# Optimization experiments

Hardware: AMD Instinct MI355X
Metric: run time of the kernel (lower is better)

Reference implementation:

```python
import jax, jax.numpy as jnp
import numpy as np

N_HEADS = 16


def setup_inputs() -> dict:
    key = jax.random.key(0)
    k1, k2, k3, k4 = jax.random.split(key, 4)
    b, s, d = 2, 2048, 1024
    x = jax.random.normal(k1, (b, s, d), dtype=jnp.float32)
    attn_B = jax.random.normal(k2, (b, N_HEADS, s, s), dtype=jnp.float32) * 0.02
    W_attn = jax.random.normal(k3, (d, 3 * d), dtype=jnp.float32) * (1.0 / np.sqrt(d))
    b_attn = jax.random.normal(k4, (3 * d,), dtype=jnp.float32) * 0.01
    return {"x": x, "attn_B": attn_B, "W_attn": W_attn, "b_attn": b_attn}


def reference(x, attn_B, W_attn, b_attn):
    b, s, d = x.shape
    h = N_HEADS
    hd = d // h
    qkv = x @ W_attn + b_attn                       # [b, s, 3d]
    Q, K, V = jnp.split(qkv, 3, axis=-1)
    # [b, s, d] -> [b, h, s, hd]
    Q = Q.reshape(b, s, h, hd).transpose(0, 2, 1, 3)
    K = K.reshape(b, s, h, hd).transpose(0, 2, 1, 3)
    V = V.reshape(b, s, h, hd).transpose(0, 2, 1, 3)
    scale = 1.0 / jnp.sqrt(jnp.asarray(hd, dtype=Q.dtype))
    scores = jnp.einsum("bhqk,bhsk->bhqs", Q, K) * scale   # [b, h, s, s]
    attn = jax.nn.softmax(scores, axis=-1) + attn_B          # post-softmax additive bias
    y = jnp.einsum("bhqs,bhsd->bhqd", attn, V)               # [b, h, s, hd]
    y = y.transpose(0, 2, 1, 3).reshape(b, s, d)
    return y
```

## Files before the change

### kernel.cpp

```cpp
#include <hip/hip_runtime.h>
#include <hip/hip_bf16.h>


typedef __attribute__((ext_vector_type(4))) float  f32x4;
typedef __attribute__((ext_vector_type(8))) short  bf16x8;
typedef __attribute__((ext_vector_type(4))) short  s16x4;

__device__ __forceinline__ short f2bf(float f) {
    __hip_bfloat16 h = __float2bfloat16(f);
    return __builtin_bit_cast(short, h);
}

__device__ __forceinline__ unsigned cvt_pk_bf16(float lo, float hi) {
    unsigned w;
    asm("v_cvt_pk_bf16_f32 %0, %1, %2" : "=v"(w) : "v"(lo), "v"(hi));
    return w;
}

__device__ __forceinline__ void gll16(const short* g, short* l) {
    __builtin_amdgcn_global_load_lds(
        (const __attribute__((address_space(1))) void*)g,
        (__attribute__((address_space(3))) void*)l, 16, 0, 0);
}

__global__ void conv_x_kernel(const float* __restrict__ x, short* __restrict__ xb) {
    int idx = blockIdx.x * 256 + threadIdx.x;
    f32x4 v = *reinterpret_cast<const f32x4*>(x + (size_t)idx * 4);
    s16x4 o;
    o[0] = f2bf(v[0]); o[1] = f2bf(v[1]); o[2] = f2bf(v[2]); o[3] = f2bf(v[3]);
    *reinterpret_cast<s16x4*>(xb + (size_t)idx * 4) = o;
}

__global__ void wtrans_kernel(const float* __restrict__ W, short* __restrict__ Wt) {
    __shared__ float tile[64][65];
    int kb = blockIdx.x, nb = blockIdx.y;
    int t = threadIdx.x;
    int c4 = (t & 15) * 4;
    int r0 = t >> 4;
#pragma unroll
    for (int rr = 0; rr < 4; ++rr) {
        int kl = r0 + rr * 16;
        f32x4 v = *reinterpret_cast<const f32x4*>(W + (size_t)(kb * 64 + kl) * 3072 + nb * 64 + c4);
        tile[kl][c4 + 0] = v[0]; tile[kl][c4 + 1] = v[1];
        tile[kl][c4 + 2] = v[2]; tile[kl][c4 + 3] = v[3];
    }
    __syncthreads();
#pragma unroll
    for (int rr = 0; rr < 4; ++rr) {
        int nl = r0 + rr * 16;
        s16x4 o;
#pragma unroll
        for (int i = 0; i < 4; ++i) o[i] = f2bf(tile[c4 + i][nl]);
        *reinterpret_cast<s16x4*>(Wt + (size_t)(nb * 64 + nl) * 1024 + kb * 64 + c4) = o;
    }
}

__global__ __launch_bounds__(256) void qkv_gemm_kernel(
    const short* __restrict__ xb, const short* __restrict__ Wt,
    const float* __restrict__ bias,
    short* __restrict__ Qo, short* __restrict__ Ko, short* __restrict__ Vo)
{
    __shared__ short As[128 * 64];
    __shared__ short Bs[128 * 64];
    int tid = threadIdx.x;
    int wave = tid >> 6, lane = tid & 63, g = lane >> 4, lr = lane & 15;
    int wr = wave >> 1, wc = wave & 1;
    int bm = blockIdx.x, bn = blockIdx.y;

    f32x4 acc[4][4];
#pragma unroll
    for (int a = 0; a < 4; ++a)
#pragma unroll
        for (int b = 0; b < 4; ++b) acc[a][b] = (f32x4){0.f, 0.f, 0.f, 0.f};

    for (int k0 = 0; k0 < 1024; k0 += 64) {
#pragma unroll
        for (int j = 0; j < 4; ++j) {
            int c = j * 256 + tid;
            int row = c >> 3, cc = c & 7;
            int scc = (cc ^ (row & 7)) * 8;
            gll16(xb + (size_t)(bm * 128 + row) * 1024 + k0 + scc,
                  &As[(j * 256 + wave * 64) * 8]);
            gll16(Wt + (size_t)(bn * 128 + row) * 1024 + k0 + scc,
                  &Bs[(j * 256 + wave * 64) * 8]);
        }
        __syncthreads();

        bf16x8 af[2][4], bfr[2][4];
#pragma unroll
        for (int mt = 0; mt < 4; ++mt) {
            int row = wr * 64 + mt * 16 + lr;
            af[0][mt] = *reinterpret_cast<const bf16x8*>(&As[row * 64 + (((g    ) ^ (lr & 7)) * 8)]);
            af[1][mt] = *reinterpret_cast<const bf16x8*>(&As[row * 64 + (((g + 4) ^ (lr & 7)) * 8)]);
        }
#pragma unroll
        for (int nt = 0; nt < 4; ++nt) {
            int row = wc * 64 + nt * 16 + lr;
            bfr[0][nt] = *reinterpret_cast<const bf16x8*>(&Bs[row * 64 + (((g    ) ^ (lr & 7)) * 8)]);
            bfr[1][nt] = *reinterpret_cast<const bf16x8*>(&Bs[row * 64 + (((g + 4) ^ (lr & 7)) * 8)]);
        }
#pragma unroll
        for (int mt = 0; mt < 4; ++mt)
#pragma unroll
            for (int nt = 0; nt < 4; ++nt) {
                acc[mt][nt] = __builtin_amdgcn_mfma_f32_16x16x32_bf16(af[0][mt], bfr[0][nt], acc[mt][nt], 0, 0, 0);
                acc[mt][nt] = __builtin_amdgcn_mfma_f32_16x16x32_bf16(af[1][mt], bfr[1][nt], acc[mt][nt], 0, 0, 0);
            }
        __syncthreads();
    }

#pragma unroll
    for (int nt = 0; nt < 4; ++nt) {
        int n = bn * 128 + wc * 64 + nt * 16 + lr;
        float bv = bias[n];
        int which = n >> 10;
        int h = (n >> 6) & 15;
        int dd = n & 63;
        short* base = (which == 0) ? Qo : (which == 1) ? Ko : Vo;
#pragma unroll
        for (int mt = 0; mt < 4; ++mt) {
#pragma unroll
            for (int r = 0; r < 4; ++r) {
                int m = bm * 128 + wr * 64 + mt * 16 + g * 4 + r;
                int bb = m >> 11, s = m & 2047;
                float v = acc[mt][nt][r] + bv;
                base[(((size_t)bb * 16 + h) * 2048 + s) * 64 + dd] = f2bf(v);
            }
        }
    }
}

__global__ __launch_bounds__(256) void vtrans_kernel(const short* __restrict__ V, short* __restrict__ Vt) {
    __shared__ short t[64][72];
    int st = blockIdx.x, bh = blockIdx.y;
    int tid = threadIdx.x;
#pragma unroll
    for (int j = 0; j < 2; ++j) {
        int c = j * 256 + tid;
        int row = c >> 3, cc = c & 7;
        bf16x8 v = *reinterpret_cast<const bf16x8*>(V + (size_t)((bh * 2048) + st * 64 + row) * 64 + cc * 8);
        *reinterpret_cast<bf16x8*>(&t[row][cc * 8]) = v;
    }
    __syncthreads();
#pragma unroll
    for (int j = 0; j < 2; ++j) {
        int c = j * 256 + tid;
        int d = c >> 3, cs = c & 7;
        bf16x8 o;
#pragma unroll
        for (int i = 0; i < 8; ++i) o[i] = t[cs * 8 + i][d];
        *reinterpret_cast<bf16x8*>(Vt + (size_t)(bh * 64 + d) * 2048 + st * 64 + cs * 8) = o;
    }
}

__global__ __launch_bounds__(256, 4) void attn_kernel(
    const short* __restrict__ Qw, const short* __restrict__ Kw, const short* __restrict__ Vtw,
    const float* __restrict__ attnB, float* __restrict__ out)
{
    __shared__ short Ks [2][64 * 64];
    __shared__ short Vts[2][64 * 64];
    __shared__ short Ps [4][16 * 64];

    int qt = blockIdx.x, bh = blockIdx.y;
    int b = bh >> 4, h = bh & 15;
    int tid = threadIdx.x;
    int wave = tid >> 6, lane = tid & 63, g = lane >> 4, lr = lane & 15;

    const short* Qb = Qw  + (size_t)bh * 2048 * 64;
    const short* Kb = Kw  + (size_t)bh * 2048 * 64;
    const short* Vb = Vtw + (size_t)bh * 64 * 2048;
    const float* Bp = attnB + (size_t)bh * 2048 * 2048;

    int qbase = qt * 64 + wave * 16;

    bf16x8 qf0, qf1;
    {
        const short* qp = Qb + (size_t)(qbase + lr) * 64 + g * 8;
        qf0 = *reinterpret_cast<const bf16x8*>(qp);
        qf1 = *reinterpret_cast<const bf16x8*>(qp + 32);
    }
    const float* brow = Bp + (size_t)(qbase + lr) * 2048 + g * 8;

    f32x4 Os[4], Ob[4];
#pragma unroll
    for (int dt = 0; dt < 4; ++dt) { Os[dt] = (f32x4){0.f,0.f,0.f,0.f}; Ob[dt] = (f32x4){0.f,0.f,0.f,0.f}; }
    float lsum = 0.f;

#define STAGE_KV(buf, ktt) do {                                                   \
    _Pragma("unroll")                                                             \
    for (int j = 0; j < 2; ++j) {                                                 \
        int c = j * 256 + tid;                                                    \
        int row = c >> 3, cc = c & 7;                                             \
        int scc = (cc ^ (row & 7)) * 8;                                           \
        gll16(Kb + (size_t)((ktt) * 64 + row) * 64 + scc,                         \
              &Ks[buf][(j * 256 + wave * 64) * 8]);                               \
        gll16(Vb + (size_t)row * 2048 + (ktt) * 64 + scc,                         \
              &Vts[buf][(j * 256 + wave * 64) * 8]);                              \
    }                                                                             \
} while (0)

    f32x4 bfn0, bfn1, bfn2, bfn3;
    STAGE_KV(0, 0);
    __builtin_amdgcn_sched_barrier(0);
    bfn0 = *reinterpret_cast<const f32x4*>(brow);
    bfn1 = *reinterpret_cast<const f32x4*>(brow + 4);
    bfn2 = *reinterpret_cast<const f32x4*>(brow + 32);
    bfn3 = *reinterpret_cast<const f32x4*>(brow + 36);
    asm volatile("s_waitcnt vmcnt(4)" ::: "memory");
    __builtin_amdgcn_s_barrier();
    __builtin_amdgcn_sched_barrier(0);

    for (int kt = 0; kt < 32; ++kt) {
        int cur = kt & 1;

        unsigned bb0 = cvt_pk_bf16(bfn0[0], bfn0[1]);
        unsigned bb1 = cvt_pk_bf16(bfn0[2], bfn0[3]);
        unsigned bb2 = cvt_pk_bf16(bfn1[0], bfn1[1]);
        unsigned bb3 = cvt_pk_bf16(bfn1[2], bfn1[3]);
        unsigned bb4 = cvt_pk_bf16(bfn2[0], bfn2[1]);
        unsigned bb5 = cvt_pk_bf16(bfn2[2], bfn2[3]);
        unsigned bb6 = cvt_pk_bf16(bfn3[0], bfn3[1]);
        unsigned bb7 = cvt_pk_bf16(bfn3[2], bfn3[3]);

        if (kt < 31) {
            STAGE_KV(cur ^ 1, kt + 1);
            __builtin_amdgcn_sched_barrier(0);
            const float* bp = brow + (kt + 1) * 64;
            bfn0 = *reinterpret_cast<const f32x4*>(bp);
            bfn1 = *reinterpret_cast<const f32x4*>(bp + 4);
            bfn2 = *reinterpret_cast<const f32x4*>(bp + 32);
            bfn3 = *reinterpret_cast<const f32x4*>(bp + 36);
        }

        f32x4 S[4];
        __builtin_amdgcn_s_setprio(1);
#pragma unroll
        for (int nt = 0; nt < 4; ++nt) {
            int row = nt * 16 + lr;
            bf16x8 kf0 = *reinterpret_cast<const bf16x8*>(&Ks[cur][row * 64 + (((g    ) ^ (lr & 7)) * 8)]);
            bf16x8 kf1 = *reinterpret_cast<const bf16x8*>(&Ks[cur][row * 64 + (((g + 4) ^ (lr & 7)) * 8)]);
            f32x4 s = (f32x4){0.f,0.f,0.f,0.f};
            s = __builtin_amdgcn_mfma_f32_16x16x32_bf16(kf0, qf0, s, 0, 0, 0);
            s = __builtin_amdgcn_mfma_f32_16x16x32_bf16(kf1, qf1, s, 0, 0, 0);
            S[nt] = s;
        }
        __builtin_amdgcn_s_setprio(0);

#pragma unroll
        for (int nt = 0; nt < 4; ++nt)
#pragma unroll
            for (int r = 0; r < 4; ++r) {
                float p = exp2f(S[nt][r] * 0.1803368801111f);
                S[nt][r] = p;
                lsum += p;
            }

        short* psw = &Ps[wave][lr * 64];
#pragma unroll
        for (int nt = 0; nt < 4; ++nt)
#pragma unroll
            for (int rp = 0; rp < 2; ++rp) {
                unsigned w = cvt_pk_bf16(S[nt][2 * rp], S[nt][2 * rp + 1]);
                int kp = 8 * nt + 2 * g + rp;
                int bi = kp >> 2, off = kp & 3;
                *reinterpret_cast<unsigned*>(psw + ((bi ^ (lr & 7)) << 3) + off * 2) = w;
            }

        bf16x8 pf0 = *reinterpret_cast<const bf16x8*>(&Ps[wave][lr * 64 + (((g    ) ^ (lr & 7)) * 8)]);
        bf16x8 pf1 = *reinterpret_cast<const bf16x8*>(&Ps[wave][lr * 64 + (((g + 4) ^ (lr & 7)) * 8)]);
        bf16x8 bbf0, bbf1;
        {
            typedef __attribute__((ext_vector_type(4))) unsigned u32x4;
            u32x4 t0 = (u32x4){bb0, bb1, bb2, bb3};
            u32x4 t1 = (u32x4){bb4, bb5, bb6, bb7};
            bbf0 = __builtin_bit_cast(bf16x8, t0);
            bbf1 = __builtin_bit_cast(bf16x8, t1);
        }

        __builtin_amdgcn_s_setprio(1);
#pragma unroll
        for (int dt = 0; dt < 4; ++dt) {
            int row = dt * 16 + lr;
            bf16x8 v0 = *reinterpret_cast<const bf16x8*>(&Vts[cur][row * 64 + (((g    ) ^ (lr & 7)) * 8)]);
            bf16x8 v1 = *reinterpret_cast<const bf16x8*>(&Vts[cur][row * 64 + (((g + 4) ^ (lr & 7)) * 8)]);
            Os[dt] = __builtin_amdgcn_mfma_f32_16x16x32_bf16(pf0,  v0, Os[dt], 0, 0, 0);
            Os[dt] = __builtin_amdgcn_mfma_f32_16x16x32_bf16(pf1,  v1, Os[dt], 0, 0, 0);
            Ob[dt] = __builtin_amdgcn_mfma_f32_16x16x32_bf16(bbf0, v0, Ob[dt], 0, 0, 0);
            Ob[dt] = __builtin_amdgcn_mfma_f32_16x16x32_bf16(bbf1, v1, Ob[dt], 0, 0, 0);
        }
        __builtin_amdgcn_s_setprio(0);

        if (kt < 31) {
            asm volatile("s_waitcnt vmcnt(4)" ::: "memory");
            __builtin_amdgcn_s_barrier();
            __builtin_amdgcn_sched_barrier(0);
        }
    }
#undef STAGE_KV

    float l = lsum;
    l += __shfl_xor(l, 16);
    l += __shfl_xor(l, 32);
    float inv = 1.0f / l;
#pragma unroll
    for (int r = 0; r < 4; ++r) {
        float invr = __shfl(inv, g * 4 + r);
        int q = qbase + g * 4 + r;
#pragma unroll
        for (int dt = 0; dt < 4; ++dt) {
            int dcol = dt * 16 + lr;
            out[((size_t)(b * 2048 + q) * 16 + h) * 64 + dcol] = Os[dt][r] * invr + Ob[dt][r];
        }
    }
}

extern "C" void kernel_launch(void* const* d_in, const int* in_sizes, int n_in,
                              void* d_out, int out_size, void* d_ws, size_t ws_size,
                              hipStream_t stream) {
    const float* x     = (const float*)d_in[0];
    const float* attnB = (const float*)d_in[1];
    const float* W     = (const float*)d_in[2];
    const float* bias  = (const float*)d_in[3];
    float* out = (float*)d_out;

    short* ws = (short*)d_ws;
    short* xb = ws;
    short* Wt = xb + 4194304;
    short* Q  = Wt + 3145728;
    short* K  = Q  + 4194304;
    short* V  = K  + 4194304;
    short* Vt = V  + 4194304;

    conv_x_kernel<<<4096, 256, 0, stream>>>(x, xb);
    wtrans_kernel<<<dim3(16, 48), 256, 0, stream>>>(W, Wt);
    qkv_gemm_kernel<<<dim3(32, 24), 256, 0, stream>>>(xb, Wt, bias, Q, K, V);
    vtrans_kernel<<<dim3(32, 32), 256, 0, stream>>>(V, Vt);
    attn_kernel<<<dim3(32, 32), 256, 0, stream>>>(Q, K, Vt, attnB, out);
}
```

Measured before the change: 206.6 us.

## Double attention block to 8 waves sharing K/V tiles, remap grid, nontemporal bias

The attention kernel now runs 512 threads (8 waves) per block covering 128 query rows, so each staged K/V tile in LDS is shared by twice as many waves and K/V global traffic halves. Block indices are remapped so that consecutive blocks interleave 8 heads, which spreads concurrent work across heads. The bias stream and output stores use nontemporal hints to avoid polluting cache. The risks are fewer blocks (512) for occupancy and higher LDS/register pressure per block under launch_bounds(512,4).

```diff
diff --git a/kernel.cpp b/kernel.cpp
--- a/kernel.cpp
+++ b/kernel.cpp
@@ -5,6 +5,7 @@
 typedef __attribute__((ext_vector_type(4))) float  f32x4;
 typedef __attribute__((ext_vector_type(8))) short  bf16x8;
 typedef __attribute__((ext_vector_type(4))) short  s16x4;
+typedef __attribute__((ext_vector_type(4))) unsigned u32x4;
 
 __device__ __forceinline__ short f2bf(float f) {
     __hip_bfloat16 h = __float2bfloat16(f);
@@ -153,15 +154,18 @@
     }
 }
 
-__global__ __launch_bounds__(256, 4) void attn_kernel(
+__global__ __launch_bounds__(512, 4) void attn_kernel(
     const short* __restrict__ Qw, const short* __restrict__ Kw, const short* __restrict__ Vtw,
     const float* __restrict__ attnB, float* __restrict__ out)
 {
     __shared__ short Ks [2][64 * 64];
     __shared__ short Vts[2][64 * 64];
-    __shared__ short Ps [4][16 * 64];
-
-    int qt = blockIdx.x, bh = blockIdx.y;
+    __shared__ short Ps [8][16 * 64];
+
+    int id = blockIdx.x;
+    int bh3 = id & 7;
+    int qt  = (id >> 3) & 15;
+    int bh  = ((id >> 7) << 3) | bh3;
     int b = bh >> 4, h = bh & 15;
     int tid = threadIdx.x;
     int wave = tid >> 6, lane = tid & 63, g = lane >> 4, lr = lane & 15;
@@ -171,7 +175,7 @@
     const short* Vb = Vtw + (size_t)bh * 64 * 2048;
     const float* Bp = attnB + (size_t)bh * 2048 * 2048;
 
-    int qbase = qt * 64 + wave * 16;
+    int qbase = qt * 128 + wave * 16;
 
     bf16x8 qf0, qf1;
     {
@@ -187,25 +191,21 @@
     float lsum = 0.f;
 
 #define STAGE_KV(buf, ktt) do {                                                   \
-    _Pragma("unroll")                                                             \
-    for (int j = 0; j < 2; ++j) {                                                 \
-        int c = j * 256 + tid;                                                    \
-        int row = c >> 3, cc = c & 7;                                             \
-        int scc = (cc ^ (row & 7)) * 8;                                           \
-        gll16(Kb + (size_t)((ktt) * 64 + row) * 64 + scc,                         \
-              &Ks[buf][(j * 256 + wave * 64) * 8]);                               \
-        gll16(Vb + (size_t)row * 2048 + (ktt) * 64 + scc,                         \
-              &Vts[buf][(j * 256 + wave * 64) * 8]);                              \
-    }                                                                             \
+    int row = tid >> 3, cc = tid & 7;                                             \
+    int scc = (cc ^ (row & 7)) * 8;                                               \
+    gll16(Kb + (size_t)((ktt) * 64 + row) * 64 + scc,                             \
+          &Ks[buf][wave * 512]);                                                  \
+    gll16(Vb + (size_t)row * 2048 + (ktt) * 64 + scc,                             \
+          &Vts[buf][wave * 512]);                                                 \
 } while (0)
 
     f32x4 bfn0, bfn1, bfn2, bfn3;
     STAGE_KV(0, 0);
     __builtin_amdgcn_sched_barrier(0);
-    bfn0 = *reinterpret_cast<const f32x4*>(brow);
-    bfn1 = *reinterpret_cast<const f32x4*>(brow + 4);
-    bfn2 = *reinterpret_cast<const f32x4*>(brow + 32);
-    bfn3 = *reinterpret_cast<const f32x4*>(brow + 36);
+    bfn0 = __builtin_nontemporal_load(reinterpret_cast<const f32x4*>(brow));
+    bfn1 = __builtin_nontemporal_load(reinterpret_cast<const f32x4*>(brow + 4));
+    bfn2 = __builtin_nontemporal_load(reinterpret_cast<const f32x4*>(brow + 32));
+    bfn3 = __builtin_nontemporal_load(reinterpret_cast<const f32x4*>(brow + 36));
     asm volatile("s_waitcnt vmcnt(4)" ::: "memory");
     __builtin_amdgcn_s_barrier();
     __builtin_amdgcn_sched_barrier(0);
@@ -226,10 +226,10 @@
             STAGE_KV(cur ^ 1, kt + 1);
             __builtin_amdgcn_sched_barrier(0);
             const float* bp = brow + (kt + 1) * 64;
-            bfn0 = *reinterpret_cast<const f32x4*>(bp);
-            bfn1 = *reinterpret_cast<const f32x4*>(bp + 4);
-            bfn2 = *reinterpret_cast<const f32x4*>(bp + 32);
-            bfn3 = *reinterpret_cast<const f32x4*>(bp + 36);
+            bfn0 = __builtin_nontemporal_load(reinterpret_cast<const f32x4*>(bp));
+            bfn1 = __builtin_nontemporal_load(reinterpret_cast<const f32x4*>(bp + 4));
+            bfn2 = __builtin_nontemporal_load(reinterpret_cast<const f32x4*>(bp + 32));
+            bfn3 = __builtin_nontemporal_load(reinterpret_cast<const f32x4*>(bp + 36));
         }
 
         f32x4 S[4];
@@ -270,7 +270,6 @@
         bf16x8 pf1 = *reinterpret_cast<const bf16x8*>(&Ps[wave][lr * 64 + (((g + 4) ^ (lr & 7)) * 8)]);
         bf16x8 bbf0, bbf1;
         {
-            typedef __attribute__((ext_vector_type(4))) unsigned u32x4;
             u32x4 t0 = (u32x4){bb0, bb1, bb2, bb3};
             u32x4 t1 = (u32x4){bb4, bb5, bb6, bb7};
             bbf0 = __builtin_bit_cast(bf16x8, t0);
@@ -309,7 +308,8 @@
 #pragma unroll
         for (int dt = 0; dt < 4; ++dt) {
             int dcol = dt * 16 + lr;
-            out[((size_t)(b * 2048 + q) * 16 + h) * 64 + dcol] = Os[dt][r] * invr + Ob[dt][r];
+            float v = Os[dt][r] * invr + Ob[dt][r];
+            __builtin_nontemporal_store(v, &out[((size_t)(b * 2048 + q) * 16 + h) * 64 + dcol]);
         }
     }
 }
@@ -335,5 +335,5 @@
     wtrans_kernel<<<dim3(16, 48), 256, 0, stream>>>(W, Wt);
     qkv_gemm_kernel<<<dim3(32, 24), 256, 0, stream>>>(xb, Wt, bias, Q, K, V);
     vtrans_kernel<<<dim3(32, 32), 256, 0, stream>>>(V, Vt);
-    attn_kernel<<<dim3(32, 32), 256, 0, stream>>>(Q, K, Vt, attnB, out);
-}
+    attn_kernel<<<512, 512, 0, stream>>>(Q, K, Vt, attnB, out);
+}
```

After: 205.5 us. Within noise of the previous version (-0.5%).
